# Kernel tuning notes

Measured on AMD Instinct MI355X. Metric: run time of the kernel, lower is better.

Reference implementation:

```python
import jax, jax.numpy as jnp
import numpy as np
from itertools import combinations

NUM_FIELDS = 32
INPUT_DIM = 64
BATCH = 4096
PAIRS = np.array(list(combinations(range(NUM_FIELDS), 2)), dtype=np.int32)  # [P, 2], P=496


def setup_inputs() -> dict:
    key = jax.random.key(0)
    k1, k2 = jax.random.split(key)
    x = jax.random.normal(k1, (BATCH, NUM_FIELDS, INPUT_DIM), dtype=jnp.float32)
    # One Linear(D, D, bias=False) weight per field pair (nn.Linear convention: y = x @ W.T)
    W = jax.random.normal(k2, (PAIRS.shape[0], INPUT_DIM, INPUT_DIM), dtype=jnp.float32) * 0.05
    return {"x": x, "W": W}


def reference(x, W) -> jnp.ndarray:
    # x: [B, F, D], W: [P, D, D] where P = C(F, 2)
    pi = jnp.asarray(PAIRS[:, 0])  # first field of each pair
    pj = jnp.asarray(PAIRS[:, 1])  # second field of each pair
    xi = x[:, pi, :]  # [B, P, D]
    xj = x[:, pj, :]  # [B, P, D]
    # Batched tiny GEMM: y_p = xi_p @ W_p.T  (nn.Linear semantics), fused with multiply
    proj = jnp.einsum('bpd,pod->bpo', xi, W)  # [B, P, D]
    return proj * xj  # concat over pairs == stacked pair dim -> [B, P, D]
```

## Files before the change

### kernel.cpp

```cpp
#include <hip/hip_runtime.h>

#define NBATCH 4096
#define NF     32
#define DIM    64
#define NPAIRS 496

#define MTILE  128
#define LDAP   72

typedef _Float16 half8  __attribute__((ext_vector_type(8)));
typedef _Float16 half4v __attribute__((ext_vector_type(4)));
typedef float    floatx4 __attribute__((ext_vector_type(4)));

__global__ __launch_bounds__(256, 4)
void bilinear_mfma(const float* __restrict__ x, const float* __restrict__ W,
                   float* __restrict__ out) {
    __shared__ _Float16 sW[DIM * LDAP];

    const int tid  = threadIdx.x;
    const int lane = tid & 63;
    const int wv   = tid >> 6;
    const int lrow = lane & 15;
    const int quad = lane >> 4;

    const int p  = blockIdx.x % NPAIRS;
    const int bt = blockIdx.x / NPAIRS;
    const int b0 = bt * MTILE;

    int fi = 0, rem = p;
    while (rem >= NF - 1 - fi) { rem -= NF - 1 - fi; ++fi; }
    const int fj = fi + 1 + rem;

    const float* Wp = W + (size_t)p * (DIM * DIM);
    #pragma unroll
    for (int it = 0; it < 4; ++it) {
        int idx = tid + 256 * it;
        int o   = idx >> 4;
        int c4  = (idx & 15) << 2;
        const floatx4 v = *(const floatx4*)(Wp + o * DIM + c4);
        half4v hv;
        hv[0] = (_Float16)v[0]; hv[1] = (_Float16)v[1];
        hv[2] = (_Float16)v[2]; hv[3] = (_Float16)v[3];
        *(half4v*)(&sW[o * LDAP + c4]) = hv;
    }

    half8 bx[2][2];
    #pragma unroll
    for (int bt2 = 0; bt2 < 2; ++bt2) {
        const int b = b0 + wv * 32 + bt2 * 16 + lrow;
        const float* xrow = x + ((size_t)b * NF + fi) * DIM;
        #pragma unroll
        for (int ks = 0; ks < 2; ++ks) {
            const floatx4 v0 = *(const floatx4*)(xrow + ks * 32 + quad * 8);
            const floatx4 v1 = *(const floatx4*)(xrow + ks * 32 + quad * 8 + 4);
            half8 h;
            h[0] = (_Float16)v0[0]; h[1] = (_Float16)v0[1];
            h[2] = (_Float16)v0[2]; h[3] = (_Float16)v0[3];
            h[4] = (_Float16)v1[0]; h[5] = (_Float16)v1[1];
            h[6] = (_Float16)v1[2]; h[7] = (_Float16)v1[3];
            bx[bt2][ks] = h;
        }
    }
    __syncthreads();

    floatx4 acc[2][4] = {};
    #pragma unroll
    for (int ks = 0; ks < 2; ++ks) {
        half8 aw[4];
        #pragma unroll
        for (int ot = 0; ot < 4; ++ot)
            aw[ot] = *(const half8*)(&sW[(ot * 16 + lrow) * LDAP + ks * 32 + quad * 8]);
        #pragma unroll
        for (int bt2 = 0; bt2 < 2; ++bt2)
            #pragma unroll
            for (int ot = 0; ot < 4; ++ot)
                acc[bt2][ot] = __builtin_amdgcn_mfma_f32_16x16x32_f16(aw[ot], bx[bt2][ks], acc[bt2][ot], 0, 0, 0);
    }

    #pragma unroll
    for (int bt2 = 0; bt2 < 2; ++bt2) {
        const size_t b = (size_t)(b0 + wv * 32 + bt2 * 16 + lrow);
        const float* xjrow = x + (b * NF + fj) * DIM;
        float* orow = out + b * (NPAIRS * DIM) + (size_t)p * DIM;
        #pragma unroll
        for (int ot = 0; ot < 4; ++ot) {
            const int o4 = ot * 16 + quad * 4;
            const floatx4 xj = *(const floatx4*)(xjrow + o4);
            const floatx4 a = acc[bt2][ot];
            floatx4 res;
            res[0] = a[0] * xj[0]; res[1] = a[1] * xj[1];
            res[2] = a[2] * xj[2]; res[3] = a[3] * xj[3];
            __builtin_nontemporal_store(res, (floatx4*)(orow + o4));
        }
    }
}

extern "C" void kernel_launch(void* const* d_in, const int* in_sizes, int n_in,
                              void* d_out, int out_size, void* d_ws, size_t ws_size,
                              hipStream_t stream) {
    const float* x = (const float*)d_in[0];
    const float* W = (const float*)d_in[1];
    float* out = (float*)d_out;

    dim3 grid(NPAIRS * (NBATCH / MTILE));
    bilinear_mfma<<<grid, 256, 0, stream>>>(x, W, out);
}
```

Baseline: 632.4 us.

## Pre-convert inputs to fp16 in workspace and load MFMA operands directly

Adds a conversion kernel that writes fp16 copies of x and W into the workspace, then runs a main kernel that loads W fragments straight from global into registers, removing the LDS staging and the block barrier, and halves the bytes of x reread per pair. The xj multiplier is now read in fp16, which adds rounding error to the elementwise product. The original kernel is kept as a fallback when the workspace is too small. The extra launch and conversion pass add memory traffic.

```diff
diff --git a/kernel.cpp b/kernel.cpp
--- a/kernel.cpp
+++ b/kernel.cpp
@@ -4,19 +4,37 @@
 #define NF     32
 #define DIM    64
 #define NPAIRS 496
+#define MTILE  128
 
-#define MTILE  128
-#define LDAP   72
+#define X_ELEMS (NBATCH * NF * DIM)
+#define W_ELEMS (NPAIRS * DIM * DIM)
+#define X_V4    (X_ELEMS / 4)
+#define TOT_V4  ((X_ELEMS + W_ELEMS) / 4)
 
 typedef _Float16 half8  __attribute__((ext_vector_type(8)));
 typedef _Float16 half4v __attribute__((ext_vector_type(4)));
 typedef float    floatx4 __attribute__((ext_vector_type(4)));
 
+__global__ __launch_bounds__(256)
+void cvt_f16(const float* __restrict__ x, const float* __restrict__ W,
+             _Float16* __restrict__ xh, _Float16* __restrict__ Wh) {
+    int idx = blockIdx.x * 256 + threadIdx.x;
+    const int stride = gridDim.x * 256;
+    for (; idx < TOT_V4; idx += stride) {
+        const float* src; _Float16* dst; int o;
+        if (idx < X_V4) { src = x; dst = xh; o = idx * 4; }
+        else            { src = W; dst = Wh; o = (idx - X_V4) * 4; }
+        const floatx4 v = *(const floatx4*)(src + o);
+        half4v h;
+        h[0] = (_Float16)v[0]; h[1] = (_Float16)v[1];
+        h[2] = (_Float16)v[2]; h[3] = (_Float16)v[3];
+        *(half4v*)(dst + o) = h;
+    }
+}
+
 __global__ __launch_bounds__(256, 4)
-void bilinear_mfma(const float* __restrict__ x, const float* __restrict__ W,
-                   float* __restrict__ out) {
-    __shared__ _Float16 sW[DIM * LDAP];
-
+void bilinear_f16(const _Float16* __restrict__ xh, const _Float16* __restrict__ Wh,
+                  float* __restrict__ out) {
     const int tid  = threadIdx.x;
     const int lane = tid & 63;
     const int wv   = tid >> 6;
@@ -31,19 +49,70 @@
     while (rem >= NF - 1 - fi) { rem -= NF - 1 - fi; ++fi; }
     const int fj = fi + 1 + rem;
 
+    const _Float16* Wp = Wh + (size_t)p * (DIM * DIM);
+    half8 aw[2][4];
+    #pragma unroll
+    for (int ks = 0; ks < 2; ++ks)
+        #pragma unroll
+        for (int ot = 0; ot < 4; ++ot)
+            aw[ks][ot] = *(const half8*)(Wp + (ot * 16 + lrow) * DIM + ks * 32 + quad * 8);
+
+    half8 bx[2][2];
+    #pragma unroll
+    for (int bt2 = 0; bt2 < 2; ++bt2) {
+        const int b = b0 + wv * 32 + bt2 * 16 + lrow;
+        const _Float16* xrow = xh + ((size_t)b * NF + fi) * DIM;
+        #pragma unroll
+        for (int ks = 0; ks < 2; ++ks)
+            bx[bt2][ks] = *(const half8*)(xrow + ks * 32 + quad * 8);
+    }
+
+    floatx4 acc[2][4] = {};
+    #pragma unroll
+    for (int ks = 0; ks < 2; ++ks)
+        #pragma unroll
+        for (int bt2 = 0; bt2 < 2; ++bt2)
+            #pragma unroll
+            for (int ot = 0; ot < 4; ++ot)
+                acc[bt2][ot] = __builtin_amdgcn_mfma_f32_16x16x32_f16(aw[ks][ot], bx[bt2][ks], acc[bt2][ot], 0, 0, 0);
+
+    #pragma unroll
+    for (int bt2 = 0; bt2 < 2; ++bt2) {
+        const size_t b = (size_t)(b0 + wv * 32 + bt2 * 16 + lrow);
+        const _Float16* xjrow = xh + (b * NF + fj) * DIM;
+        float* orow = out + b * (NPAIRS * DIM) + (size_t)p * DIM;
+        #pragma unroll
+        for (int ot = 0; ot < 4; ++ot) {
+            const int o4 = ot * 16 + quad * 4;
+            const half4v xj = *(const half4v*)(xjrow + o4);
+            const floatx4 a = acc[bt2][ot];
+            floatx4 res;
+            res[0] = a[0] * (float)xj[0]; res[1] = a[1] * (float)xj[1];
+            res[2] = a[2] * (float)xj[2]; res[3] = a[3] * (float)xj[3];
+            __builtin_nontemporal_store(res, (floatx4*)(orow + o4));
+        }
+    }
+}
+
+#define LDAP 72
+__global__ __launch_bounds__(256, 4)
+void bilinear_fb(const float* __restrict__ x, const float* __restrict__ W,
+                 float* __restrict__ out) {
+    __shared__ _Float16 sW[DIM * LDAP];
+    const int tid = threadIdx.x, lane = tid & 63, wv = tid >> 6;
+    const int lrow = lane & 15, quad = lane >> 4;
+    const int p = blockIdx.x % NPAIRS, bt = blockIdx.x / NPAIRS, b0 = bt * MTILE;
+    int fi = 0, rem = p;
+    while (rem >= NF - 1 - fi) { rem -= NF - 1 - fi; ++fi; }
+    const int fj = fi + 1 + rem;
     const float* Wp = W + (size_t)p * (DIM * DIM);
     #pragma unroll
     for (int it = 0; it < 4; ++it) {
-        int idx = tid + 256 * it;
-        int o   = idx >> 4;
-        int c4  = (idx & 15) << 2;
+        int idx = tid + 256 * it, o = idx >> 4, c4 = (idx & 15) << 2;
         const floatx4 v = *(const floatx4*)(Wp + o * DIM + c4);
-        half4v hv;
-        hv[0] = (_Float16)v[0]; hv[1] = (_Float16)v[1];
-        hv[2] = (_Float16)v[2]; hv[3] = (_Float16)v[3];
+        half4v hv; hv[0]=(_Float16)v[0]; hv[1]=(_Float16)v[1]; hv[2]=(_Float16)v[2]; hv[3]=(_Float16)v[3];
         *(half4v*)(&sW[o * LDAP + c4]) = hv;
     }
-
     half8 bx[2][2];
     #pragma unroll
     for (int bt2 = 0; bt2 < 2; ++bt2) {
@@ -54,15 +123,12 @@
             const floatx4 v0 = *(const floatx4*)(xrow + ks * 32 + quad * 8);
             const floatx4 v1 = *(const floatx4*)(xrow + ks * 32 + quad * 8 + 4);
             half8 h;
-            h[0] = (_Float16)v0[0]; h[1] = (_Float16)v0[1];
-            h[2] = (_Float16)v0[2]; h[3] = (_Float16)v0[3];
-            h[4] = (_Float16)v1[0]; h[5] = (_Float16)v1[1];
-            h[6] = (_Float16)v1[2]; h[7] = (_Float16)v1[3];
+            h[0]=(_Float16)v0[0]; h[1]=(_Float16)v0[1]; h[2]=(_Float16)v0[2]; h[3]=(_Float16)v0[3];
+            h[4]=(_Float16)v1[0]; h[5]=(_Float16)v1[1]; h[6]=(_Float16)v1[2]; h[7]=(_Float16)v1[3];
             bx[bt2][ks] = h;
         }
     }
     __syncthreads();
-
     floatx4 acc[2][4] = {};
     #pragma unroll
     for (int ks = 0; ks < 2; ++ks) {
@@ -76,7 +142,6 @@
             for (int ot = 0; ot < 4; ++ot)
                 acc[bt2][ot] = __builtin_amdgcn_mfma_f32_16x16x32_f16(aw[ot], bx[bt2][ks], acc[bt2][ot], 0, 0, 0);
     }
-
     #pragma unroll
     for (int bt2 = 0; bt2 < 2; ++bt2) {
         const size_t b = (size_t)(b0 + wv * 32 + bt2 * 16 + lrow);
@@ -88,8 +153,7 @@
             const floatx4 xj = *(const floatx4*)(xjrow + o4);
             const floatx4 a = acc[bt2][ot];
             floatx4 res;
-            res[0] = a[0] * xj[0]; res[1] = a[1] * xj[1];
-            res[2] = a[2] * xj[2]; res[3] = a[3] * xj[3];
+            res[0]=a[0]*xj[0]; res[1]=a[1]*xj[1]; res[2]=a[2]*xj[2]; res[3]=a[3]*xj[3];
             __builtin_nontemporal_store(res, (floatx4*)(orow + o4));
         }
     }
@@ -102,6 +166,15 @@
     const float* W = (const float*)d_in[1];
     float* out = (float*)d_out;
 
+    const size_t need = (size_t)(X_ELEMS + W_ELEMS) * sizeof(_Float16);
     dim3 grid(NPAIRS * (NBATCH / MTILE));
-    bilinear_mfma<<<grid, 256, 0, stream>>>(x, W, out);
+
+    if (ws_size >= need) {
+        _Float16* xh = (_Float16*)d_ws;
+        _Float16* Wh = xh + X_ELEMS;
+        cvt_f16<<<dim3(2048), 256, 0, stream>>>(x, W, xh, Wh);
+        bilinear_f16<<<grid, 256, 0, stream>>>(xh, Wh, out);
+    } else {
+        bilinear_fb<<<grid, 256, 0, stream>>>(x, W, out);
+    }
 }
```

Measured after the change: 611.9 us. 1.03x faster.
